# Kernel tuning notes

Hardware: AMD Instinct MI355X
Metric: run time of the kernel (lower is better)

Reference implementation:

```python
import jax, jax.numpy as jnp
import numpy as np

B_, C_, H_, W_ = 4, 256, 64, 64
D_MODEL = C_ // 4        # 64, mamba d_model
D_INNER = 2 * D_MODEL    # 128, expand=2
D_STATE = 16
D_CONV = 4
DT_RANK = 4              # ceil(d_model/16)


def setup_inputs() -> dict:
    key = jax.random.key(0)
    ks = jax.random.split(key, 10)
    s = 0.02
    p = {}
    p["x"] = jax.random.normal(ks[0], (B_, C_, H_, W_), jnp.float32)
    p["norm_g"] = jnp.ones((C_,), jnp.float32)
    p["norm_b"] = jnp.zeros((C_,), jnp.float32)
    p["skip_scale"] = jnp.ones((1,), jnp.float32)
    p["proj_w"] = jax.random.normal(ks[1], (C_, C_), jnp.float32) * s
    p["proj_b"] = jnp.zeros((C_,), jnp.float32)
    p["in_proj_w"] = jax.random.normal(ks[2], (2 * D_INNER, D_MODEL), jnp.float32) * s
    p["conv_w"] = jax.random.normal(ks[3], (D_INNER, 1, D_CONV), jnp.float32) * s
    p["conv_b"] = jnp.zeros((D_INNER,), jnp.float32)
    p["x_proj_w"] = jax.random.normal(ks[4], (DT_RANK + 2 * D_STATE, D_INNER), jnp.float32) * s
    p["dt_w"] = jax.random.normal(ks[5], (D_INNER, DT_RANK), jnp.float32) * s
    p["dt_b"] = jax.random.normal(ks[6], (D_INNER,), jnp.float32) * 0.1
    # S4D-real init: A_n = n for n in 1..d_state
    p["A_log"] = jnp.log(jnp.broadcast_to(jnp.arange(1, D_STATE + 1, dtype=jnp.float32), (D_INNER, D_STATE)))
    p["D"] = jnp.ones((D_INNER,), jnp.float32)
    p["out_w"] = jax.random.normal(ks[7], (D_MODEL, D_INNER), jnp.float32) * s
    return p


def _layernorm(x, g, b, eps=1e-5):
    mu = jnp.mean(x, axis=-1, keepdims=True)
    var = jnp.mean(jnp.square(x - mu), axis=-1, keepdims=True)
    return (x - mu) * jax.lax.rsqrt(var + eps) * g + b


def _mamba(x, in_proj_w, conv_w, conv_b, x_proj_w, dt_w, dt_b, A_log, D, out_w):
    # x: [N, L, d_model]
    N, L, _ = x.shape
    xz = x @ in_proj_w.T                      # [N, L, 2*d_inner]
    xi, z = jnp.split(xz, 2, axis=-1)
    # causal depthwise conv1d over time
    xc = jax.lax.conv_general_dilated(
        xi.transpose(0, 2, 1), conv_w, (1,), [(D_CONV - 1, 0)],
        feature_group_count=D_INNER)          # [N, d_inner, L]
    u = jax.nn.silu((xc + conv_b[None, :, None]).transpose(0, 2, 1))  # [N, L, d_inner]
    dbl = u @ x_proj_w.T                      # [N, L, dt_rank + 2*d_state]
    dt, Bm, Cm = jnp.split(dbl, [DT_RANK, DT_RANK + D_STATE], axis=-1)
    delta = jax.nn.softplus(dt @ dt_w.T + dt_b)  # [N, L, d_inner]
    A = -jnp.exp(A_log)                       # [d_inner, d_state]

    def step(h, inp):
        d_t, B_t, C_t, u_t = inp              # [N,d], [N,n], [N,n], [N,d]
        dA = jnp.exp(d_t[:, :, None] * A)     # [N, d, n]
        h = dA * h + (d_t * u_t)[:, :, None] * B_t[:, None, :]
        y = jnp.einsum('bdn,bn->bd', h, C_t)
        return h, y

    h0 = jnp.zeros((N, D_INNER, D_STATE), x.dtype)
    xs = (delta.transpose(1, 0, 2), Bm.transpose(1, 0, 2),
          Cm.transpose(1, 0, 2), u.transpose(1, 0, 2))
    _, ys = jax.lax.scan(step, h0, xs)        # ys: [L, N, d_inner]
    y = ys.transpose(1, 0, 2) + u * D
    y = y * jax.nn.silu(z)
    return y @ out_w.T                        # [N, L, d_model]


def reference(x, norm_g, norm_b, skip_scale, proj_w, proj_b, in_proj_w, conv_w,
              conv_b, x_proj_w, dt_w, dt_b, A_log, D, out_w):
    B, C = x.shape[:2]
    img_dims = x.shape[2:]
    xf = x.reshape(B, C, -1).transpose(0, 2, 1)       # [B, L, C]
    xn = _layernorm(xf, norm_g, norm_b)
    parts = jnp.split(xn, 8, axis=2)
    b1 = jnp.concatenate([parts[7], parts[0]], axis=2)
    b2 = jnp.concatenate([parts[1], parts[2]], axis=2)
    b3 = jnp.concatenate([parts[3], parts[4]], axis=2)
    b4 = jnp.concatenate([parts[5], parts[6]], axis=2)
    # if_shifted_round=True: all four branches share the same mamba -> batch them
    stacked = jnp.concatenate([b1, b2, b3, b4], axis=0)  # [4B, L, C/4]
    ym = _mamba(stacked, in_proj_w, conv_w, conv_b, x_proj_w,
                dt_w, dt_b, A_log, D, out_w) + skip_scale * stacked
    m1, m2, m3, m4 = jnp.split(ym, 4, axis=0)
    t8, t1 = jnp.split(m1, 2, axis=2)
    xm = jnp.concatenate([t1, m2, m3, m4, t8], axis=2)   # [B, L, C]
    xm = _layernorm(xm, norm_g, norm_b)
    xm = xm @ proj_w.T + proj_b
    return xm.transpose(0, 2, 1).reshape(B, -1, *img_dims)
```

## Files before the change

kernel.cpp:

```cpp
#include <hip/hip_runtime.h>
#include <hip/hip_bf16.h>

#define L_ 4096
#define CCH 256
#define CH 64
#define NC 64

__global__ __launch_bounds__(256) void k1_ln_scatter(
    const float* __restrict__ x, const float* __restrict__ g,
    const float* __restrict__ bb, float* __restrict__ stacked) {
  int b = blockIdx.y;
  int l0 = blockIdx.x * 64;
  int t = threadIdx.x;
  int lane = t & 63, w = t >> 6;
  __shared__ float xs[256][65];
  __shared__ float ps[4][64], ps2[4][64];
  __shared__ float mean_s[64], rstd_s[64];
  for (int i = 0; i < 64; ++i) {
    int c = w + 4 * i;
    xs[c][lane] = x[((size_t)b * 256 + c) * L_ + l0 + lane];
  }
  __syncthreads();
  float sum = 0.f, sq = 0.f;
  for (int c = w * 64; c < w * 64 + 64; ++c) {
    float v = xs[c][lane];
    sum += v; sq += v * v;
  }
  ps[w][lane] = sum; ps2[w][lane] = sq;
  __syncthreads();
  if (w == 0) {
    float s = ps[0][lane] + ps[1][lane] + ps[2][lane] + ps[3][lane];
    float q = ps2[0][lane] + ps2[1][lane] + ps2[2][lane] + ps2[3][lane];
    float mean = s * (1.f / 256.f);
    mean_s[lane] = mean;
    rstd_s[lane] = rsqrtf(q * (1.f / 256.f) - mean * mean + 1e-5f);
  }
  __syncthreads();
  int br = w, j = lane;
  int c = (br * 64 + j + 224) & 255;
  float gv = g[c], bv = bb[c];
  float* dst = stacked + ((size_t)(br * 4 + b) * L_ + l0) * 64 + j;
  for (int l = 0; l < 64; ++l) {
    float v = (xs[c][l] - mean_s[l]) * rstd_s[l] * gv + bv;
    dst[(size_t)l * 64] = v;
  }
}

__global__ __launch_bounds__(256) void k2_inproj(
    const float* __restrict__ stacked, const float* __restrict__ w,
    float* __restrict__ xi, float* __restrict__ z) {
  int n = blockIdx.z, l0 = blockIdx.x * 64, k0 = blockIdx.y * 64;
  __shared__ float As[64][68];
  __shared__ float Ws[64][68];
  int t = threadIdx.y * 16 + threadIdx.x;
  for (int e = t; e < 4096; e += 256) {
    int r = e >> 6, c = e & 63;
    As[r][c] = stacked[((size_t)n * L_ + l0 + r) * 64 + c];
    Ws[r][c] = w[(k0 + r) * 64 + c];
  }
  __syncthreads();
  float acc[4][4] = {};
  for (int jj = 0; jj < 16; ++jj) {
    float4 a[4], bm[4];
#pragma unroll
    for (int i = 0; i < 4; i++) a[i] = *reinterpret_cast<const float4*>(&As[threadIdx.y * 4 + i][jj * 4]);
#pragma unroll
    for (int i = 0; i < 4; i++) bm[i] = *reinterpret_cast<const float4*>(&Ws[threadIdx.x * 4 + i][jj * 4]);
#pragma unroll
    for (int i = 0; i < 4; i++)
#pragma unroll
      for (int kk = 0; kk < 4; kk++)
        acc[i][kk] += a[i].x * bm[kk].x + a[i].y * bm[kk].y + a[i].z * bm[kk].z + a[i].w * bm[kk].w;
  }
  int kb = k0 + threadIdx.x * 4;
  float* dst = (kb < 128) ? xi : z;
  int kd = (kb < 128) ? kb : kb - 128;
#pragma unroll
  for (int i = 0; i < 4; i++) {
    int l = l0 + threadIdx.y * 4 + i;
    float4 v = make_float4(acc[i][0], acc[i][1], acc[i][2], acc[i][3]);
    *reinterpret_cast<float4*>(&dst[((size_t)n * L_ + l) * 128 + kd]) = v;
  }
}

__global__ __launch_bounds__(256) void k3_conv_xproj(
    const float* __restrict__ xi, const float* __restrict__ cw,
    const float* __restrict__ cb, const float* __restrict__ xw,
    const float* __restrict__ dtw, const float* __restrict__ dtb,
    float* __restrict__ u, float* __restrict__ delta,
    float* __restrict__ Bc, float* __restrict__ Cc) {
  int n = blockIdx.y, l0 = blockIdx.x * 64;
  int tid = threadIdx.x;
  __shared__ float us[64][129];
  __shared__ float dbls[64][37];

  {
    int d = tid & 127, lh = tid >> 7;
    int ls = l0 + lh * 32;
    const float* xp = xi + ((size_t)n * L_ + ls) * 128 + d;
    const float4 cwv = *reinterpret_cast<const float4*>(&cw[d * 4]);
    float cbv = cb[d];
    float xm3 = (ls >= 3) ? xp[-3 * 128] : 0.f;
    float xm2 = (ls >= 2) ? xp[-2 * 128] : 0.f;
    float xm1 = (ls >= 1) ? xp[-1 * 128] : 0.f;
    float* up = u + ((size_t)n * L_ + ls) * 128 + d;
#pragma unroll 4
    for (int l = 0; l < 32; ++l) {
      float xv = xp[(size_t)l * 128];
      float s = cbv + cwv.x * xm3 + cwv.y * xm2 + cwv.z * xm1 + cwv.w * xv;
      float uv = s / (1.f + __expf(-s));
      us[lh * 32 + l][d] = uv;
      up[(size_t)l * 128] = uv;
      xm3 = xm2; xm2 = xm1; xm1 = xv;
    }
  }
  __syncthreads();

  {
    int l = tid & 63, q = tid >> 6;
    float acc[9] = {};
    for (int d = 0; d < 128; ++d) {
      float uv = us[l][d];
#pragma unroll
      for (int r = 0; r < 9; ++r) acc[r] += uv * xw[(q * 9 + r) * 128 + d];
    }
#pragma unroll
    for (int r = 0; r < 9; ++r) dbls[l][q * 9 + r] = acc[r];
  }
  __syncthreads();

  {
    int d = tid & 127, lh = tid >> 7;
    const float4 wv = *reinterpret_cast<const float4*>(&dtw[d * 4]);
    float bv = dtb[d];
    float* dp = delta + ((size_t)n * L_ + l0 + lh * 32) * 128 + d;
    for (int l = 0; l < 32; ++l) {
      int lr = lh * 32 + l;
      float q0 = dbls[lr][0], q1 = dbls[lr][1], q2 = dbls[lr][2], q3 = dbls[lr][3];
      float dv = bv + q0 * wv.x + q1 * wv.y + q2 * wv.z + q3 * wv.w;
      dv = (dv > 20.f) ? dv : log1pf(__expf(dv));
      dp[(size_t)l * 128] = dv;
    }
  }

  {
    int s = tid & 15;
    int which = (tid >> 4) & 1;
    int lg = tid >> 5;
    float* dst = which ? Cc : Bc;
    int roff = 4 + which * 16 + s;
    for (int l3 = lg; l3 < 64; l3 += 8) {
      dst[((size_t)n * L_ + l0 + l3) * 16 + s] = dbls[l3][roff];
    }
  }
}

__global__ __launch_bounds__(128) void k4a_chunk(
    const float* __restrict__ delta, const float* __restrict__ u,
    const float* __restrict__ Bc, const float* __restrict__ A_log,
    float* __restrict__ hend, float* __restrict__ Sdelta) {
  int c = blockIdx.x, n = blockIdx.y, d = threadIdx.x;
  __shared__ float Bs[CH * 16];
  const float* bsrc = Bc + ((size_t)n * L_ + c * CH) * 16;
  for (int e = d; e < CH * 16; e += 128) Bs[e] = bsrc[e];
  float A[16];
#pragma unroll
  for (int s = 0; s < 16; ++s) A[s] = -__expf(A_log[d * 16 + s]);
  __syncthreads();

  const float* dp = delta + ((size_t)n * L_ + c * CH) * 128 + d;
  const float* up = u + ((size_t)n * L_ + c * CH) * 128 + d;
  float h[16] = {};
  float sd = 0.f;
  float dv = dp[0], uv = up[0];
  for (int l = 0; l < CH; ++l) {
    int ln = (l + 1 < CH) ? l + 1 : l;
    float dvn = dp[(size_t)ln * 128];
    float uvn = up[(size_t)ln * 128];
    sd += dv;
    float du = dv * uv;
    float bsv[16];
    *reinterpret_cast<float4*>(&bsv[0])  = *reinterpret_cast<const float4*>(&Bs[l * 16 + 0]);
    *reinterpret_cast<float4*>(&bsv[4])  = *reinterpret_cast<const float4*>(&Bs[l * 16 + 4]);
    *reinterpret_cast<float4*>(&bsv[8])  = *reinterpret_cast<const float4*>(&Bs[l * 16 + 8]);
    *reinterpret_cast<float4*>(&bsv[12]) = *reinterpret_cast<const float4*>(&Bs[l * 16 + 12]);
#pragma unroll
    for (int s = 0; s < 16; ++s)
      h[s] = fmaf(__expf(dv * A[s]), h[s], du * bsv[s]);
    dv = dvn; uv = uvn;
  }
  float* hp = hend + (((size_t)n * NC + c) * 128 + d) * 16;
  *reinterpret_cast<float4*>(&hp[0])  = make_float4(h[0], h[1], h[2], h[3]);
  *reinterpret_cast<float4*>(&hp[4])  = make_float4(h[4], h[5], h[6], h[7]);
  *reinterpret_cast<float4*>(&hp[8])  = make_float4(h[8], h[9], h[10], h[11]);
  *reinterpret_cast<float4*>(&hp[12]) = make_float4(h[12], h[13], h[14], h[15]);
  Sdelta[((size_t)n * NC + c) * 128 + d] = sd;
}

__global__ __launch_bounds__(256) void k4b_combine(
    const float* __restrict__ Sdelta, const float* __restrict__ A_log,
    float* __restrict__ hend) {
  int n = blockIdx.x >> 3, d0 = (blockIdx.x & 7) * 16;
  int d = d0 + (threadIdx.x >> 4), s = threadIdx.x & 15;
  float A = -__expf(A_log[d * 16 + s]);
  float H = 0.f;
  size_t i0 = ((size_t)n * NC) * 128 + d;
  float sd = Sdelta[i0];
  float he = hend[i0 * 16 + s];
  for (int c = 0; c < NC; ++c) {
    int cn = (c + 1 < NC) ? c + 1 : c;
    size_t in_ = ((size_t)n * NC + cn) * 128 + d;
    float sdn = Sdelta[in_];
    float hen = hend[in_ * 16 + s];
    size_t i = ((size_t)n * NC + c) * 128 + d;
    hend[i * 16 + s] = H;
    H = fmaf(__expf(A * sd), H, he);
    sd = sdn; he = hen;
  }
}

__global__ __launch_bounds__(256) void k45_scan_gate_proj(
    const float* __restrict__ delta, const float* __restrict__ u,
    const float* __restrict__ Bc, const float* __restrict__ Cc,
    const float* __restrict__ A_log, const float* __restrict__ Hstart,
    const float* __restrict__ z, const float* __restrict__ Dv,
    const float* __restrict__ ow, const float* __restrict__ stacked,
    const float* __restrict__ skip, float* __restrict__ ym) {
  int c = blockIdx.x, n = blockIdx.y;
  int tid = threadIdx.x;
  __shared__ float As[64][132];
  __shared__ float Ws[64][132];
  __shared__ float Bs[CH * 16];
  __shared__ float Cs[CH * 16];

  const float* bsrc = Bc + ((size_t)n * L_ + c * CH) * 16;
  const float* csrc = Cc + ((size_t)n * L_ + c * CH) * 16;
  for (int e = tid; e < CH * 16; e += 256) { Bs[e] = bsrc[e]; Cs[e] = csrc[e]; }
  for (int e = tid; e < 64 * 128; e += 256) {
    int r = e >> 7, d = e & 127;
    Ws[r][d] = ow[(size_t)r * 128 + d];
  }
  __syncthreads();

  if (tid < 128) {
    int d = tid;
    float A[16];
#pragma unroll
    for (int s = 0; s < 16; ++s) A[s] = -__expf(A_log[d * 16 + s]);
    const float* hp = Hstart + (((size_t)n * NC + c) * 128 + d) * 16;
    float h[16];
    *reinterpret_cast<float4*>(&h[0])  = *reinterpret_cast<const float4*>(&hp[0]);
    *reinterpret_cast<float4*>(&h[4])  = *reinterpret_cast<const float4*>(&hp[4]);
    *reinterpret_cast<float4*>(&h[8])  = *reinterpret_cast<const float4*>(&hp[8]);
    *reinterpret_cast<float4*>(&h[12]) = *reinterpret_cast<const float4*>(&hp[12]);
    const float* dp = delta + ((size_t)n * L_ + c * CH) * 128 + d;
    const float* up = u + ((size_t)n * L_ + c * CH) * 128 + d;
    const float* zp = z + ((size_t)n * L_ + c * CH) * 128 + d;
    float Dd = Dv[d];
    float dv = dp[0], uv = up[0], zv = zp[0];
    for (int l = 0; l < CH; ++l) {
      int ln = (l + 1 < CH) ? l + 1 : l;
      float dvn = dp[(size_t)ln * 128];
      float uvn = up[(size_t)ln * 128];
      float zvn = zp[(size_t)ln * 128];
      float du = dv * uv;
      float bsv[16], csv[16];
      *reinterpret_cast<float4*>(&bsv[0])  = *reinterpret_cast<const float4*>(&Bs[l * 16 + 0]);
      *reinterpret_cast<float4*>(&bsv[4])  = *reinterpret_cast<const float4*>(&Bs[l * 16 + 4]);
      *reinterpret_cast<float4*>(&bsv[8])  = *reinterpret_cast<const float4*>(&Bs[l * 16 + 8]);
      *reinterpret_cast<float4*>(&bsv[12]) = *reinterpret_cast<const float4*>(&Bs[l * 16 + 12]);
      *reinterpret_cast<float4*>(&csv[0])  = *reinterpret_cast<const float4*>(&Cs[l * 16 + 0]);
      *reinterpret_cast<float4*>(&csv[4])  = *reinterpret_cast<const float4*>(&Cs[l * 16 + 4]);
      *reinterpret_cast<float4*>(&csv[8])  = *reinterpret_cast<const float4*>(&Cs[l * 16 + 8]);
      *reinterpret_cast<float4*>(&csv[12]) = *reinterpret_cast<const float4*>(&Cs[l * 16 + 12]);
      float yv = 0.f;
#pragma unroll
      for (int s = 0; s < 16; ++s) {
        h[s] = fmaf(__expf(dv * A[s]), h[s], du * bsv[s]);
        yv = fmaf(h[s], csv[s], yv);
      }
      As[l][d] = (yv + uv * Dd) * (zv / (1.f + __expf(-zv)));
      dv = dvn; uv = uvn; zv = zvn;
    }
  }
  __syncthreads();

  int tx = tid & 15, ty = tid >> 4;
  float acc[4][4] = {};
  for (int jj = 0; jj < 32; ++jj) {
    float4 a[4], bm[4];
#pragma unroll
    for (int i = 0; i < 4; i++) a[i] = *reinterpret_cast<const float4*>(&As[ty * 4 + i][jj * 4]);
#pragma unroll
    for (int i = 0; i < 4; i++) bm[i] = *reinterpret_cast<const float4*>(&Ws[tx * 4 + i][jj * 4]);
#pragma unroll
    for (int i = 0; i < 4; i++)
#pragma unroll
      for (int kk = 0; kk < 4; kk++)
        acc[i][kk] += a[i].x * bm[kk].x + a[i].y * bm[kk].y + a[i].z * bm[kk].z + a[i].w * bm[kk].w;
  }
  float sk = skip[0];
  int l0 = c * CH;
#pragma unroll
  for (int i = 0; i < 4; i++) {
    int l = l0 + ty * 4 + i;
    const float4 st = *reinterpret_cast<const float4*>(&stacked[((size_t)n * L_ + l) * 64 + tx * 4]);
    float4 v = make_float4(acc[i][0] + sk * st.x, acc[i][1] + sk * st.y,
                           acc[i][2] + sk * st.z, acc[i][3] + sk * st.w);
    *reinterpret_cast<float4*>(&ym[((size_t)n * L_ + l) * 64 + tx * 4]) = v;
  }
}

__global__ __launch_bounds__(256) void k6_ln_proj(
    const float* __restrict__ ym, const float* __restrict__ g,
    const float* __restrict__ bb, const float* __restrict__ pw,
    const float* __restrict__ pb, float* __restrict__ out) {
  int b = blockIdx.z, k0 = blockIdx.y * 64, l0 = blockIdx.x * 64;
  __shared__ float As[64][68];
  __shared__ float Ws[64][68];
  __shared__ float mean_s[64], rstd_s[64];
  int t = threadIdx.y * 16 + threadIdx.x;
  int lane = t & 63, w = t >> 6;

  for (int li = w; li < 64; li += 4) {
    int l = l0 + li;
    float sum = 0.f, sq = 0.f;
#pragma unroll
    for (int br = 0; br < 4; ++br) {
      float v = ym[((size_t)(br * 4 + b) * L_ + l) * 64 + lane];
      sum += v; sq += v * v;
    }
#pragma unroll
    for (int off = 1; off < 64; off <<= 1) {
      sum += __shfl_xor(sum, off);
      sq  += __shfl_xor(sq, off);
    }
    if (lane == 0) {
      float mean = sum * (1.f / 256.f);
      mean_s[li] = mean;
      rstd_s[li] = rsqrtf(sq * (1.f / 256.f) - mean * mean + 1e-5f);
    }
  }
  __syncthreads();

  float acc[4][4] = {};
  for (int cc = 0; cc < 4; ++cc) {
    __syncthreads();
    for (int e = t; e < 4096; e += 256) {
      int r = e >> 6, cj = e & 63;
      int ch = cc * 64 + cj;
      int gi = (ch + 32) & 255;
      int br = gi >> 6, j = gi & 63;
      float v = ym[((size_t)(br * 4 + b) * L_ + l0 + r) * 64 + j];
      As[r][cj] = (v - mean_s[r]) * rstd_s[r] * g[ch] + bb[ch];
      Ws[r][cj] = pw[(k0 + r) * 256 + ch];
    }
    __syncthreads();
    for (int jj = 0; jj < 16; ++jj) {
      float4 a[4], bm[4];
#pragma unroll
      for (int i = 0; i < 4; i++) a[i] = *reinterpret_cast<const float4*>(&As[threadIdx.y * 4 + i][jj * 4]);
#pragma unroll
      for (int i = 0; i < 4; i++) bm[i] = *reinterpret_cast<const float4*>(&Ws[threadIdx.x * 4 + i][jj * 4]);
#pragma unroll
      for (int i = 0; i < 4; i++)
#pragma unroll
        for (int kk = 0; kk < 4; kk++)
          acc[i][kk] += a[i].x * bm[kk].x + a[i].y * bm[kk].y + a[i].z * bm[kk].z + a[i].w * bm[kk].w;
    }
  }
  __syncthreads();
  float* Ct = &As[0][0];
#pragma unroll
  for (int i = 0; i < 4; i++)
#pragma unroll
    for (int kk = 0; kk < 4; kk++)
      Ct[(threadIdx.y * 4 + i) * 65 + (threadIdx.x * 4 + kk)] = acc[i][kk];
  __syncthreads();
#pragma unroll
  for (int p = 0; p < 16; ++p) {
    int row = p * 4 + w;
    out[((size_t)b * 256 + k0 + row) * L_ + l0 + lane] = Ct[lane * 65 + row] + pb[k0 + row];
  }
}

extern "C" void kernel_launch(void* const* d_in, const int* in_sizes, int n_in,
                              void* d_out, int out_size, void* d_ws, size_t ws_size,
                              hipStream_t stream) {
  const float* x        = (const float*)d_in[0];
  const float* norm_g   = (const float*)d_in[1];
  const float* norm_b   = (const float*)d_in[2];
  const float* skip     = (const float*)d_in[3];
  const float* proj_w   = (const float*)d_in[4];
  const float* proj_b   = (const float*)d_in[5];
  const float* in_proj_w= (const float*)d_in[6];
  const float* conv_w   = (const float*)d_in[7];
  const float* conv_b   = (const float*)d_in[8];
  const float* x_proj_w = (const float*)d_in[9];
  const float* dt_w     = (const float*)d_in[10];
  const float* dt_b     = (const float*)d_in[11];
  const float* A_log    = (const float*)d_in[12];
  const float* Dv       = (const float*)d_in[13];
  const float* out_w    = (const float*)d_in[14];
  float* out = (float*)d_out;
  float* ws  = (float*)d_ws;

  float* stacked = ws;
  float* xi      = ws + 4194304;
  float* z       = ws + 12582912;
  float* u       = ws + 20971520;
  float* delta   = ws + 29360128;
  float* Bc      = ws + 37748736;
  float* Cc      = ws + 38797312;
  float* ym      = xi;

  float* hend   = out;
  float* Sdelta = out + 2097152;

  k1_ln_scatter<<<dim3(64, 4), 256, 0, stream>>>(x, norm_g, norm_b, stacked);
  k2_inproj<<<dim3(64, 4, 16), dim3(16, 16), 0, stream>>>(stacked, in_proj_w, xi, z);
  k3_conv_xproj<<<dim3(64, 16), 256, 0, stream>>>(xi, conv_w, conv_b, x_proj_w,
                                                  dt_w, dt_b, u, delta, Bc, Cc);
  k4a_chunk<<<dim3(NC, 16), 128, 0, stream>>>(delta, u, Bc, A_log, hend, Sdelta);
  k4b_combine<<<128, 256, 0, stream>>>(Sdelta, A_log, hend);
  k45_scan_gate_proj<<<dim3(NC, 16), 256, 0, stream>>>(delta, u, Bc, Cc, A_log, hend,
                                                       z, Dv, out_w, stacked, skip, ym);
  k6_ln_proj<<<dim3(64, 4, 4), dim3(16, 16), 0, stream>>>(ym, norm_g, norm_b,
                                                          proj_w, proj_b, out);
}
```

Before: 414.1 us.

## Split SSM state across thread pairs in chunk scans and retune smem padding

The chunked scan kernels (k4a_chunk and the fused scan/gate/projection kernel) now give each channel two threads, each owning 8 of the 16 state elements. The partial y contributions are combined with a lane-pair shuffle. This doubles the threads working on the latency-bound sequential scan and lets all 256 threads in the fused kernel take part instead of half idling. Shared-memory row padding also changes from 68/132 to 69/133 floats. That breaks the 16-byte alignment of the float4 LDS reads in the GEMM tiles, which could cause split or slower accesses.

```diff
diff --git a/kernel.cpp b/kernel.cpp
--- a/kernel.cpp
+++ b/kernel.cpp
@@ -50,8 +50,8 @@
     const float* __restrict__ stacked, const float* __restrict__ w,
     float* __restrict__ xi, float* __restrict__ z) {
   int n = blockIdx.z, l0 = blockIdx.x * 64, k0 = blockIdx.y * 64;
-  __shared__ float As[64][68];
-  __shared__ float Ws[64][68];
+  __shared__ float As[64][69];
+  __shared__ float Ws[64][69];
   int t = threadIdx.y * 16 + threadIdx.x;
   for (int e = t; e < 4096; e += 256) {
     int r = e >> 6, c = e & 63;
@@ -155,22 +155,24 @@
   }
 }
 
-__global__ __launch_bounds__(128) void k4a_chunk(
+__global__ __launch_bounds__(256) void k4a_chunk(
     const float* __restrict__ delta, const float* __restrict__ u,
     const float* __restrict__ Bc, const float* __restrict__ A_log,
     float* __restrict__ hend, float* __restrict__ Sdelta) {
-  int c = blockIdx.x, n = blockIdx.y, d = threadIdx.x;
+  int c = blockIdx.x, n = blockIdx.y;
+  int tid = threadIdx.x;
+  int d = tid >> 1, half = tid & 1;
   __shared__ float Bs[CH * 16];
   const float* bsrc = Bc + ((size_t)n * L_ + c * CH) * 16;
-  for (int e = d; e < CH * 16; e += 128) Bs[e] = bsrc[e];
-  float A[16];
-#pragma unroll
-  for (int s = 0; s < 16; ++s) A[s] = -__expf(A_log[d * 16 + s]);
+  for (int e = tid; e < CH * 16; e += 256) Bs[e] = bsrc[e];
+  float A[8];
+#pragma unroll
+  for (int s = 0; s < 8; ++s) A[s] = -__expf(A_log[d * 16 + half * 8 + s]);
   __syncthreads();
 
   const float* dp = delta + ((size_t)n * L_ + c * CH) * 128 + d;
   const float* up = u + ((size_t)n * L_ + c * CH) * 128 + d;
-  float h[16] = {};
+  float h[8] = {};
   float sd = 0.f;
   float dv = dp[0], uv = up[0];
   for (int l = 0; l < CH; ++l) {
@@ -179,22 +181,18 @@
     float uvn = up[(size_t)ln * 128];
     sd += dv;
     float du = dv * uv;
-    float bsv[16];
-    *reinterpret_cast<float4*>(&bsv[0])  = *reinterpret_cast<const float4*>(&Bs[l * 16 + 0]);
-    *reinterpret_cast<float4*>(&bsv[4])  = *reinterpret_cast<const float4*>(&Bs[l * 16 + 4]);
-    *reinterpret_cast<float4*>(&bsv[8])  = *reinterpret_cast<const float4*>(&Bs[l * 16 + 8]);
-    *reinterpret_cast<float4*>(&bsv[12]) = *reinterpret_cast<const float4*>(&Bs[l * 16 + 12]);
-#pragma unroll
-    for (int s = 0; s < 16; ++s)
+    float bsv[8];
+    *reinterpret_cast<float4*>(&bsv[0]) = *reinterpret_cast<const float4*>(&Bs[l * 16 + half * 8]);
+    *reinterpret_cast<float4*>(&bsv[4]) = *reinterpret_cast<const float4*>(&Bs[l * 16 + half * 8 + 4]);
+#pragma unroll
+    for (int s = 0; s < 8; ++s)
       h[s] = fmaf(__expf(dv * A[s]), h[s], du * bsv[s]);
     dv = dvn; uv = uvn;
   }
-  float* hp = hend + (((size_t)n * NC + c) * 128 + d) * 16;
-  *reinterpret_cast<float4*>(&hp[0])  = make_float4(h[0], h[1], h[2], h[3]);
-  *reinterpret_cast<float4*>(&hp[4])  = make_float4(h[4], h[5], h[6], h[7]);
-  *reinterpret_cast<float4*>(&hp[8])  = make_float4(h[8], h[9], h[10], h[11]);
-  *reinterpret_cast<float4*>(&hp[12]) = make_float4(h[12], h[13], h[14], h[15]);
-  Sdelta[((size_t)n * NC + c) * 128 + d] = sd;
+  float* hp = hend + (((size_t)n * NC + c) * 128 + d) * 16 + half * 8;
+  *reinterpret_cast<float4*>(&hp[0]) = make_float4(h[0], h[1], h[2], h[3]);
+  *reinterpret_cast<float4*>(&hp[4]) = make_float4(h[4], h[5], h[6], h[7]);
+  if (half == 0) Sdelta[((size_t)n * NC + c) * 128 + d] = sd;
 }
 
 __global__ __launch_bounds__(256) void k4b_combine(
@@ -228,8 +226,8 @@
     const float* __restrict__ skip, float* __restrict__ ym) {
   int c = blockIdx.x, n = blockIdx.y;
   int tid = threadIdx.x;
-  __shared__ float As[64][132];
-  __shared__ float Ws[64][132];
+  __shared__ float As[64][133];
+  __shared__ float Ws[64][133];
   __shared__ float Bs[CH * 16];
   __shared__ float Cs[CH * 16];
 
@@ -237,22 +235,20 @@
   const float* csrc = Cc + ((size_t)n * L_ + c * CH) * 16;
   for (int e = tid; e < CH * 16; e += 256) { Bs[e] = bsrc[e]; Cs[e] = csrc[e]; }
   for (int e = tid; e < 64 * 128; e += 256) {
-    int r = e >> 7, d = e & 127;
-    Ws[r][d] = ow[(size_t)r * 128 + d];
-  }
-  __syncthreads();
-
-  if (tid < 128) {
-    int d = tid;
-    float A[16];
-#pragma unroll
-    for (int s = 0; s < 16; ++s) A[s] = -__expf(A_log[d * 16 + s]);
-    const float* hp = Hstart + (((size_t)n * NC + c) * 128 + d) * 16;
-    float h[16];
-    *reinterpret_cast<float4*>(&h[0])  = *reinterpret_cast<const float4*>(&hp[0]);
-    *reinterpret_cast<float4*>(&h[4])  = *reinterpret_cast<const float4*>(&hp[4]);
-    *reinterpret_cast<float4*>(&h[8])  = *reinterpret_cast<const float4*>(&hp[8]);
-    *reinterpret_cast<float4*>(&h[12]) = *reinterpret_cast<const float4*>(&hp[12]);
+    int r = e >> 7, dd = e & 127;
+    Ws[r][dd] = ow[(size_t)r * 128 + dd];
+  }
+  __syncthreads();
+
+  {
+    int d = tid >> 1, half = tid & 1;
+    float A[8];
+#pragma unroll
+    for (int s = 0; s < 8; ++s) A[s] = -__expf(A_log[d * 16 + half * 8 + s]);
+    const float* hp = Hstart + (((size_t)n * NC + c) * 128 + d) * 16 + half * 8;
+    float h[8];
+    *reinterpret_cast<float4*>(&h[0]) = *reinterpret_cast<const float4*>(&hp[0]);
+    *reinterpret_cast<float4*>(&h[4]) = *reinterpret_cast<const float4*>(&hp[4]);
     const float* dp = delta + ((size_t)n * L_ + c * CH) * 128 + d;
     const float* up = u + ((size_t)n * L_ + c * CH) * 128 + d;
     const float* zp = z + ((size_t)n * L_ + c * CH) * 128 + d;
@@ -264,22 +260,20 @@
       float uvn = up[(size_t)ln * 128];
       float zvn = zp[(size_t)ln * 128];
       float du = dv * uv;
-      float bsv[16], csv[16];
-      *reinterpret_cast<float4*>(&bsv[0])  = *reinterpret_cast<const float4*>(&Bs[l * 16 + 0]);
-      *reinterpret_cast<float4*>(&bsv[4])  = *reinterpret_cast<const float4*>(&Bs[l * 16 + 4]);
-      *reinterpret_cast<float4*>(&bsv[8])  = *reinterpret_cast<const float4*>(&Bs[l * 16 + 8]);
-      *reinterpret_cast<float4*>(&bsv[12]) = *reinterpret_cast<const float4*>(&Bs[l * 16 + 12]);
-      *reinterpret_cast<float4*>(&csv[0])  = *reinterpret_cast<const float4*>(&Cs[l * 16 + 0]);
-      *reinterpret_cast<float4*>(&csv[4])  = *reinterpret_cast<const float4*>(&Cs[l * 16 + 4]);
-      *reinterpret_cast<float4*>(&csv[8])  = *reinterpret_cast<const float4*>(&Cs[l * 16 + 8]);
-      *reinterpret_cast<float4*>(&csv[12]) = *reinterpret_cast<const float4*>(&Cs[l * 16 + 12]);
+      float bsv[8], csv[8];
+      *reinterpret_cast<float4*>(&bsv[0]) = *reinterpret_cast<const float4*>(&Bs[l * 16 + half * 8]);
+      *reinterpret_cast<float4*>(&bsv[4]) = *reinterpret_cast<const float4*>(&Bs[l * 16 + half * 8 + 4]);
+      *reinterpret_cast<float4*>(&csv[0]) = *reinterpret_cast<const float4*>(&Cs[l * 16 + half * 8]);
+      *reinterpret_cast<float4*>(&csv[4]) = *reinterpret_cast<const float4*>(&Cs[l * 16 + half * 8 + 4]);
       float yv = 0.f;
 #pragma unroll
-      for (int s = 0; s < 16; ++s) {
+      for (int s = 0; s < 8; ++s) {
         h[s] = fmaf(__expf(dv * A[s]), h[s], du * bsv[s]);
         yv = fmaf(h[s], csv[s], yv);
       }
-      As[l][d] = (yv + uv * Dd) * (zv / (1.f + __expf(-zv)));
+      yv += __shfl_xor(yv, 1);
+      if (half == 0)
+        As[l][d] = (yv + uv * Dd) * (zv / (1.f + __expf(-zv)));
       dv = dvn; uv = uvn; zv = zvn;
     }
   }
@@ -316,8 +310,8 @@
     const float* __restrict__ bb, const float* __restrict__ pw,
     const float* __restrict__ pb, float* __restrict__ out) {
   int b = blockIdx.z, k0 = blockIdx.y * 64, l0 = blockIdx.x * 64;
-  __shared__ float As[64][68];
-  __shared__ float Ws[64][68];
+  __shared__ float As[64][69];
+  __shared__ float Ws[64][69];
   __shared__ float mean_s[64], rstd_s[64];
   int t = threadIdx.y * 16 + threadIdx.x;
   int lane = t & 63, w = t >> 6;
@@ -421,7 +415,7 @@
   k2_inproj<<<dim3(64, 4, 16), dim3(16, 16), 0, stream>>>(stacked, in_proj_w, xi, z);
   k3_conv_xproj<<<dim3(64, 16), 256, 0, stream>>>(xi, conv_w, conv_b, x_proj_w,
                                                   dt_w, dt_b, u, delta, Bc, Cc);
-  k4a_chunk<<<dim3(NC, 16), 128, 0, stream>>>(delta, u, Bc, A_log, hend, Sdelta);
+  k4a_chunk<<<dim3(NC, 16), 256, 0, stream>>>(delta, u, Bc, A_log, hend, Sdelta);
   k4b_combine<<<128, 256, 0, stream>>>(Sdelta, A_log, hend);
   k45_scan_gate_proj<<<dim3(NC, 16), 256, 0, stream>>>(delta, u, Bc, Cc, A_log, hend,
                                                        z, Dv, out_w, stacked, skip, ym);
```

After: 393.9 us. 4.9% less time.
